# Optimization experiments

Measured on AMD Instinct MI355X. Metric: run time of the kernel, lower is better.

Reference implementation:

```python
import jax, jax.numpy as jnp
import numpy as np

D_MODEL = 1024
H = 16
DK = 64
DV = 64
D_OUT = 1024
SEQ = 1024
BATCH = 4


def setup_inputs() -> dict:
    key = jax.random.key(0)
    ks = jax.random.split(key, 11)
    s = 0.02
    return {
        "query": jax.random.normal(ks[0], (SEQ, BATCH, D_MODEL), jnp.float32),
        "key": jax.random.normal(ks[1], (SEQ, BATCH, D_MODEL), jnp.float32),
        "value": jax.random.normal(ks[2], (SEQ, BATCH, D_MODEL), jnp.float32),
        "Wq": jax.random.normal(ks[3], (D_MODEL, H * DK), jnp.float32) * s,
        "bq": jnp.zeros((H * DK,), jnp.float32),
        "Wk": jax.random.normal(ks[4], (D_MODEL, H * DK), jnp.float32) * s,
        "bk": jnp.zeros((H * DK,), jnp.float32),
        "Wv": jax.random.normal(ks[5], (D_MODEL, H * DV), jnp.float32) * s,
        "bv": jnp.zeros((H * DV,), jnp.float32),
        "Wo": jax.random.normal(ks[6], (H * DV, D_OUT), jnp.float32) * s,
        "bo": jnp.zeros((D_OUT,), jnp.float32),
    }


def reference(query, key, value, Wq, bq, Wk, bk, Wv, bv, Wo, bo):
    S, B, _ = query.shape
    # projections (seq-first layout, like the torch module)
    q = query @ Wq + bq            # (S, B, H*DK)
    k = key @ Wk + bk              # (S, B, H*DK)
    v = value @ Wv + bv            # (S, B, H*DV)
    # view + transpose(0, 2): (S, B, H, d) -> (H, B, S, d)
    q = jnp.transpose(q.reshape(S, B, H, DK), (2, 1, 0, 3))
    k = jnp.transpose(k.reshape(S, B, H, DK), (2, 1, 0, 3))
    v = jnp.transpose(v.reshape(S, B, H, DV), (2, 1, 0, 3))
    # scaled dot-product attention, full logits materialized as in the original
    logits = jnp.einsum("hbsd,hbtd->hbst", q, k) / jnp.sqrt(jnp.float32(DK))
    attn = jax.nn.softmax(logits, axis=-1)            # (H, B, S, S)
    ctx = jnp.einsum("hbst,hbtd->hbsd", attn, v)       # (H, B, S, DV)
    # transpose(0, 2) back and merge heads: (S, B, H*DV)
    ctx = jnp.transpose(ctx, (2, 1, 0, 3)).reshape(S, B, H * DV)
    out = ctx @ Wo + bo                               # (S, B, D_OUT)
    return (out, attn)
```

## Files before the change

kernel.cpp:

```cpp
#include <hip/hip_runtime.h>


typedef unsigned short u16;
typedef unsigned int u32;
typedef short short8v __attribute__((ext_vector_type(8)));
typedef short short4v __attribute__((ext_vector_type(4)));
typedef float f32x4 __attribute__((ext_vector_type(4)));

__device__ __forceinline__ u16 f2bf(float f) {
    u32 u = __builtin_bit_cast(u32, f);
    u += 0x7fffu + ((u >> 16) & 1u);
    return (u16)(u >> 16);
}
__device__ __forceinline__ f32x4 mfma_bf16(short8v a, short8v b, f32x4 c) {
    return __builtin_amdgcn_mfma_f32_16x16x32_bf16(a, b, c, 0, 0, 0);
}
__device__ __forceinline__ void gload16(const void* g, void* l) {
    __builtin_amdgcn_global_load_lds((const __attribute__((address_space(1))) u32*)g,
                                     (__attribute__((address_space(3))) u32*)l, 16, 0, 0);
}

__global__ __launch_bounds__(256) void cvt_inputs(const float* __restrict__ X0,
                                                  const float* __restrict__ X1,
                                                  const float* __restrict__ X2,
                                                  u16* __restrict__ Y0, u16* __restrict__ Y1,
                                                  u16* __restrict__ Y2) {
    const float* X; u16* Y;
    switch (blockIdx.y) {
        case 0: X = X0; Y = Y0; break;
        case 1: X = X1; Y = Y1; break;
        default: X = X2; Y = Y2; break;
    }
    const int tid = blockIdx.x * 256 + threadIdx.x;
    const int row = tid >> 7;
    const int c = tid & 127;
    const float4* s4 = reinterpret_cast<const float4*>(X + (size_t)row * 1024 + c * 8);
    float4 v0 = s4[0], v1 = s4[1];
    short8v p;
    p[0] = (short)f2bf(v0.x); p[1] = (short)f2bf(v0.y);
    p[2] = (short)f2bf(v0.z); p[3] = (short)f2bf(v0.w);
    p[4] = (short)f2bf(v1.x); p[5] = (short)f2bf(v1.y);
    p[6] = (short)f2bf(v1.z); p[7] = (short)f2bf(v1.w);
    const int dc = (c & ~7) | ((c ^ row) & 7);
    *reinterpret_cast<short8v*>(Y + (size_t)row * 1024 + dc * 8) = p;
}

__global__ __launch_bounds__(256) void cvt_transpose_w4(const float* __restrict__ W0,
                                                        const float* __restrict__ W1,
                                                        const float* __restrict__ W2,
                                                        const float* __restrict__ W3,
                                                        u16* __restrict__ T0, u16* __restrict__ T1,
                                                        u16* __restrict__ T2, u16* __restrict__ T3) {
    __shared__ u16 T[64][72];
    const float* W; u16* Wt;
    switch (blockIdx.y) {
        case 0: W = W0; Wt = T0; break;
        case 1: W = W1; Wt = T1; break;
        case 2: W = W2; Wt = T2; break;
        default: W = W3; Wt = T3; break;
    }
    const int n0 = (blockIdx.x & 15) << 6;
    const int k0 = (blockIdx.x >> 4) << 6;
    const int t = threadIdx.x;
    const int r = t >> 2;
    const int c = t & 3;
    const float4* src = reinterpret_cast<const float4*>(W + (size_t)(k0 + r) * 1024 + n0 + c * 16);
#pragma unroll
    for (int j = 0; j < 4; ++j) {
        float4 v = src[j];
        T[c * 16 + j * 4 + 0][r] = f2bf(v.x);
        T[c * 16 + j * 4 + 1][r] = f2bf(v.y);
        T[c * 16 + j * 4 + 2][r] = f2bf(v.z);
        T[c * 16 + j * 4 + 3][r] = f2bf(v.w);
    }
    __syncthreads();
    const int s = r & 7;
    const int p0 = (c << 1) ^ s;
    const int p1 = ((c << 1) | 1) ^ s;
    u16* base = Wt + (size_t)(n0 + r) * 1024 + k0;
    *reinterpret_cast<short8v*>(base + p0 * 8) = *reinterpret_cast<const short8v*>(&T[r][c * 16]);
    *reinterpret_cast<short8v*>(base + p1 * 8) = *reinterpret_cast<const short8v*>(&T[r][c * 16 + 8]);
}

__global__ __launch_bounds__(256, 3) void gemm_qkv(const u16* __restrict__ Abq,
                                                   const u16* __restrict__ Abk,
                                                   const u16* __restrict__ Abv,
                                                   const u16* __restrict__ Wtq,
                                                   const u16* __restrict__ Wtk,
                                                   const u16* __restrict__ Wtv,
                                                   const float* __restrict__ bq,
                                                   const float* __restrict__ bk,
                                                   const float* __restrict__ bv,
                                                   u16* __restrict__ dq, u16* __restrict__ dk,
                                                   u16* __restrict__ dv) {
    __shared__ u16 As[128][64];
    __shared__ u16 Bs[128][64];
    const u16* Ab; const u16* Wt; const float* bias; u16* dst;
    switch (blockIdx.z) {
        case 0: Ab = Abq; Wt = Wtq; bias = bq; dst = dq; break;
        case 1: Ab = Abk; Wt = Wtk; bias = bk; dst = dk; break;
        default: Ab = Abv; Wt = Wtv; bias = bv; dst = dv; break;
    }
    const int m0 = blockIdx.y << 7;
    const int n0 = blockIdx.x << 7;
    const int t = threadIdx.x;
    const int lane = t & 63;
    const int w = t >> 6;
    const int wr = (w >> 1) << 6;
    const int wc = (w & 1) << 6;
    const int l15 = lane & 15, lg = lane >> 4;

    const u16* ga = Ab + (size_t)(m0 + w * 32 + (lane >> 3)) * 1024 + (lane & 7) * 8;
    const u16* gb = Wt + (size_t)(n0 + w * 32 + (lane >> 3)) * 1024 + (lane & 7) * 8;

    f32x4 acc[4][4] = {};

    for (int kt = 0; kt < 16; ++kt) {
        const int k0 = kt << 6;
        if (kt) __syncthreads();
#pragma unroll
        for (int j = 0; j < 4; ++j) {
            gload16(ga + j * 8 * 1024 + k0, &As[w * 32 + j * 8][0]);
            gload16(gb + j * 8 * 1024 + k0, &Bs[w * 32 + j * 8][0]);
        }
        __syncthreads();
#pragma unroll
        for (int kk = 0; kk < 2; ++kk) {
            short8v a[4], b[4];
#pragma unroll
            for (int m = 0; m < 4; ++m) {
                const int row = wr + m * 16 + l15;
                a[m] = *reinterpret_cast<const short8v*>(&As[row][(((kk << 2) | lg) ^ (row & 7)) << 3]);
            }
#pragma unroll
            for (int n = 0; n < 4; ++n) {
                const int row = wc + n * 16 + l15;
                b[n] = *reinterpret_cast<const short8v*>(&Bs[row][(((kk << 2) | lg) ^ (row & 7)) << 3]);
            }
#pragma unroll
            for (int m = 0; m < 4; ++m)
#pragma unroll
                for (int n = 0; n < 4; ++n)
                    acc[m][n] = mfma_bf16(a[m], b[n], acc[m][n]);
        }
    }

#pragma unroll
    for (int n = 0; n < 4; ++n) {
        const int c = n0 + wc + n * 16 + l15;
        const float bvv = bias[c];
        const int h = c >> 6, d = c & 63;
#pragma unroll
        for (int m = 0; m < 4; ++m) {
#pragma unroll
            for (int r = 0; r < 4; ++r) {
                const int mi = m0 + wr + m * 16 + lg * 4 + r;
                const int s = mi >> 2, bb = mi & 3;
                dst[(size_t)(((h << 2) + bb) << 16) + (s << 6) + d] = f2bf(acc[m][n][r] + bvv);
            }
        }
    }
}

__global__ __launch_bounds__(256) void transpose_v(const u16* __restrict__ vb,
                                                   u16* __restrict__ vtb) {
    __shared__ u16 T[64][72];
    const int hb = blockIdx.y;
    const int s0 = blockIdx.x << 6;
    const u16* src = vb + (size_t)hb * 65536;
    u16* dst = vtb + (size_t)hb * 65536;
    const int t = threadIdx.x;
    const int r = t >> 2;
    const int c = (t & 3) << 4;
    short8v v0 = *reinterpret_cast<const short8v*>(src + (size_t)(s0 + r) * 64 + c);
    short8v v1 = *reinterpret_cast<const short8v*>(src + (size_t)(s0 + r) * 64 + c + 8);
#pragma unroll
    for (int j = 0; j < 8; ++j) T[c + j][r] = (u16)v0[j];
#pragma unroll
    for (int j = 0; j < 8; ++j) T[c + 8 + j][r] = (u16)v1[j];
    __syncthreads();
    *reinterpret_cast<short8v*>(dst + (size_t)r * 1024 + s0 + c)     = *reinterpret_cast<const short8v*>(&T[r][c]);
    *reinterpret_cast<short8v*>(dst + (size_t)r * 1024 + s0 + c + 8) = *reinterpret_cast<const short8v*>(&T[r][c + 8]);
}

__global__ __launch_bounds__(512, 4) void attn_kernel(const u16* __restrict__ qb,
                                                      const u16* __restrict__ kb,
                                                      const u16* __restrict__ vtb,
                                                      float* __restrict__ attn_out,
                                                      u16* __restrict__ ctxb) {
    __shared__ float Sm[16 * 1024];
    char* Sb = (char*)Sm;
    const int hb = blockIdx.y;
    const int q0 = blockIdx.x << 4;
    const int h = hb >> 2, b = hb & 3;
    const int t = threadIdx.x;
    const int lane = t & 63, w = t >> 6;
    const int l15 = lane & 15, lg = lane >> 4;

    const u16* Q = qb + (size_t)hb * 65536;
    const u16* K = kb + (size_t)hb * 65536;
    const u16* VT = vtb + (size_t)hb * 65536;

    short8v aq[2];
#pragma unroll
    for (int kh = 0; kh < 2; ++kh)
        aq[kh] = *reinterpret_cast<const short8v*>(Q + (q0 + l15) * 64 + kh * 32 + lg * 8);

#pragma unroll
    for (int n = 0; n < 8; ++n) {
        const int tcol = w * 128 + n * 16 + l15;
        f32x4 acc = {};
#pragma unroll
        for (int kh = 0; kh < 2; ++kh) {
            short8v bk = *reinterpret_cast<const short8v*>(K + tcol * 64 + kh * 32 + lg * 8);
            acc = mfma_bf16(aq[kh], bk, acc);
        }
#pragma unroll
        for (int r = 0; r < 4; ++r) {
            const int row = lg * 4 + r;
            *(float*)(Sb + (row << 12) + ((tcol << 2) ^ ((row & 7) << 4))) = acc[r] * 0.125f;
        }
    }
    __syncthreads();

#pragma unroll
    for (int rr = 0; rr < 2; ++rr) {
        const int r = w * 2 + rr;
        const int swz = (r & 7) << 4;
        f32x4 vv[4];
#pragma unroll
        for (int j = 0; j < 4; ++j)
            vv[j] = *(const f32x4*)(Sb + (r << 12) + (((lane * 4 + j * 256) << 2) ^ swz));
        float mx = -1e30f;
#pragma unroll
        for (int j = 0; j < 4; ++j)
#pragma unroll
            for (int i = 0; i < 4; ++i) mx = fmaxf(mx, vv[j][i]);
#pragma unroll
        for (int o = 1; o < 64; o <<= 1) mx = fmaxf(mx, __shfl_xor(mx, o, 64));
        float sum = 0.f;
#pragma unroll
        for (int j = 0; j < 4; ++j)
#pragma unroll
            for (int i = 0; i < 4; ++i) { vv[j][i] = __expf(vv[j][i] - mx); sum += vv[j][i]; }
#pragma unroll
        for (int o = 1; o < 64; o <<= 1) sum += __shfl_xor(sum, o, 64);
        const float inv = 1.0f / sum;
        float* grow = attn_out + (((size_t)(hb << 10) + q0 + r) << 10);
#pragma unroll
        for (int j = 0; j < 4; ++j) {
            f32x4 p = vv[j] * inv;
            *reinterpret_cast<f32x4*>(grow + lane * 4 + j * 256) = p;
            short4v pk;
            pk[0] = (short)f2bf(p[0]); pk[1] = (short)f2bf(p[1]);
            pk[2] = (short)f2bf(p[2]); pk[3] = (short)f2bf(p[3]);
            *(short4v*)(Sb + (r << 12) + (((lane * 4 + j * 256) << 1) ^ swz)) = pk;
        }
    }
    __syncthreads();

    f32x4 cacc[4] = {};
#pragma unroll
    for (int kt = 0; kt < 4; ++kt) {
        const int kcol = w * 128 + kt * 32 + lg * 8;
        short8v ap = *(const short8v*)(Sb + (l15 << 12) + ((kcol << 1) ^ ((l15 & 7) << 4)));
#pragma unroll
        for (int n = 0; n < 4; ++n) {
            short8v bv = *reinterpret_cast<const short8v*>(VT + (size_t)(n * 16 + l15) * 1024 + kcol);
            cacc[n] = mfma_bf16(ap, bv, cacc[n]);
        }
    }
    __syncthreads();

    float* part = Sm;
#pragma unroll
    for (int n = 0; n < 4; ++n)
#pragma unroll
        for (int r = 0; r < 4; ++r)
            part[w * 1088 + (lg * 4 + r) * 68 + n * 16 + l15] = cacc[n][r];
    __syncthreads();
    if (t < 256) {
        const int rrow = t >> 4;
        const int c0 = (t & 15) << 2;
        f32x4 s = {};
#pragma unroll
        for (int ww = 0; ww < 8; ++ww)
            s += *reinterpret_cast<const f32x4*>(&part[ww * 1088 + rrow * 68 + c0]);
        short4v o;
        o[0] = (short)f2bf(s[0]); o[1] = (short)f2bf(s[1]);
        o[2] = (short)f2bf(s[2]); o[3] = (short)f2bf(s[3]);
        const int mi = ((q0 + rrow) << 2) + b;
        const int off = h * 64 + (((c0 >> 3) ^ (mi & 7)) << 3) + (c0 & 7);
        *reinterpret_cast<short4v*>(ctxb + (size_t)mi * 1024 + off) = o;
    }
}

__global__ __launch_bounds__(256, 2) void gemm_out(const u16* __restrict__ ctxb,
                                                   const u16* __restrict__ Wto,
                                                   const float* __restrict__ bo,
                                                   float* __restrict__ out) {
    __shared__ u16 As[64][64];
    __shared__ u16 Bs[128][64];
    const int m0 = blockIdx.y << 6;
    const int n0 = blockIdx.x << 7;
    const int t = threadIdx.x;
    const int lane = t & 63;
    const int w = t >> 6;
    const int wr = (w >> 1) << 5;
    const int wc = (w & 1) << 6;
    const int l15 = lane & 15, lg = lane >> 4;

    const u16* ga = ctxb + (size_t)(m0 + w * 16 + (lane >> 3)) * 1024 + (lane & 7) * 8;
    const u16* gb = Wto + (size_t)(n0 + w * 32 + (lane >> 3)) * 1024 + (lane & 7) * 8;

    f32x4 acc[2][4] = {};

    for (int kt = 0; kt < 16; ++kt) {
        const int k0 = kt << 6;
        if (kt) __syncthreads();
#pragma unroll
        for (int j = 0; j < 2; ++j)
            gload16(ga + j * 8 * 1024 + k0, &As[w * 16 + j * 8][0]);
#pragma unroll
        for (int j = 0; j < 4; ++j)
            gload16(gb + j * 8 * 1024 + k0, &Bs[w * 32 + j * 8][0]);
        __syncthreads();
#pragma unroll
        for (int kk = 0; kk < 2; ++kk) {
            short8v a[2], b[4];
#pragma unroll
            for (int m = 0; m < 2; ++m) {
                const int row = wr + m * 16 + l15;
                a[m] = *reinterpret_cast<const short8v*>(&As[row][(((kk << 2) | lg) ^ (row & 7)) << 3]);
            }
#pragma unroll
            for (int n = 0; n < 4; ++n) {
                const int row = wc + n * 16 + l15;
                b[n] = *reinterpret_cast<const short8v*>(&Bs[row][(((kk << 2) | lg) ^ (row & 7)) << 3]);
            }
#pragma unroll
            for (int m = 0; m < 2; ++m)
#pragma unroll
                for (int n = 0; n < 4; ++n)
                    acc[m][n] = mfma_bf16(a[m], b[n], acc[m][n]);
        }
    }

#pragma unroll
    for (int n = 0; n < 4; ++n) {
        const int c = n0 + wc + n * 16 + l15;
        const float bvv = bo[c];
#pragma unroll
        for (int m = 0; m < 2; ++m)
#pragma unroll
            for (int r = 0; r < 4; ++r) {
                const int mi = m0 + wr + m * 16 + lg * 4 + r;
                out[(size_t)mi * 1024 + c] = acc[m][n][r] + bvv;
            }
    }
}

extern "C" void kernel_launch(void* const* d_in, const int* in_sizes, int n_in,
                              void* d_out, int out_size, void* d_ws, size_t ws_size,
                              hipStream_t stream) {
    const float* query = (const float*)d_in[0];
    const float* key   = (const float*)d_in[1];
    const float* value = (const float*)d_in[2];
    const float* Wq = (const float*)d_in[3];
    const float* bq = (const float*)d_in[4];
    const float* Wk = (const float*)d_in[5];
    const float* bk = (const float*)d_in[6];
    const float* Wv = (const float*)d_in[7];
    const float* bv = (const float*)d_in[8];
    const float* Wo = (const float*)d_in[9];
    const float* bo = (const float*)d_in[10];

    char* ws = (char*)d_ws;
    u16* Wtq  = (u16*)(ws);
    u16* Wtk  = (u16*)(ws + ((size_t)2 << 20));
    u16* Wtv  = (u16*)(ws + ((size_t)4 << 20));
    u16* Wto  = (u16*)(ws + ((size_t)6 << 20));
    u16* qb   = (u16*)(ws + ((size_t)8 << 20));
    u16* kb   = (u16*)(ws + ((size_t)16 << 20));
    u16* vb   = (u16*)(ws + ((size_t)24 << 20));
    u16* vtb  = (u16*)(ws + ((size_t)32 << 20));
    u16* ctxb = (u16*)(ws + ((size_t)24 << 20));
    u16* Abq  = (u16*)(ws + ((size_t)40 << 20));
    u16* Abk  = (u16*)(ws + ((size_t)48 << 20));
    u16* Abv  = (u16*)(ws + ((size_t)56 << 20));

    float* out  = (float*)d_out;
    float* attn = out + (size_t)4 * 1024 * 1024;

    cvt_transpose_w4<<<dim3(256, 4), 256, 0, stream>>>(Wq, Wk, Wv, Wo, Wtq, Wtk, Wtv, Wto);
    cvt_inputs<<<dim3(2048, 3), 256, 0, stream>>>(query, key, value, Abq, Abk, Abv);

    gemm_qkv<<<dim3(8, 32, 3), 256, 0, stream>>>(Abq, Abk, Abv, Wtq, Wtk, Wtv,
                                                 bq, bk, bv, qb, kb, vb);

    transpose_v<<<dim3(16, 64), 256, 0, stream>>>(vb, vtb);

    attn_kernel<<<dim3(64, 64), 512, 0, stream>>>(qb, kb, vtb, attn, ctxb);

    gemm_out<<<dim3(8, 64), 256, 0, stream>>>(ctxb, Wto, bo, out);
}
```

Measured before the change: 504.5 us.

## Split attention into QK-softmax kernel and separate tiled P·V GEMM

The fused attention kernel is split in two. The first kernel computes logits and softmax, writes the fp32 attention output, and also writes a bf16 copy of P to global memory with a swizzled layout. A new tiled GEMM kernel then computes P·V using LDS tiles with 128-row reuse, instead of each 16-row block re-reading all of V^T from global memory and doing a cross-wave reduction. The cost is an extra 128MB bf16 round trip for P and one more kernel launch, in exchange for better V reuse and lower LDS pressure in the softmax kernel.

```diff
diff --git a/kernel.cpp b/kernel.cpp
--- a/kernel.cpp
+++ b/kernel.cpp
@@ -179,27 +179,28 @@
 #pragma unroll
     for (int j = 0; j < 8; ++j) T[c + 8 + j][r] = (u16)v1[j];
     __syncthreads();
-    *reinterpret_cast<short8v*>(dst + (size_t)r * 1024 + s0 + c)     = *reinterpret_cast<const short8v*>(&T[r][c]);
-    *reinterpret_cast<short8v*>(dst + (size_t)r * 1024 + s0 + c + 8) = *reinterpret_cast<const short8v*>(&T[r][c + 8]);
-}
-
-__global__ __launch_bounds__(512, 4) void attn_kernel(const u16* __restrict__ qb,
-                                                      const u16* __restrict__ kb,
-                                                      const u16* __restrict__ vtb,
-                                                      float* __restrict__ attn_out,
-                                                      u16* __restrict__ ctxb) {
+    const int r7 = r & 7;
+    const int ch0 = (s0 + c) >> 3;
+    const int d0 = (ch0 & ~7) | ((ch0 ^ r7) & 7);
+    const int d1 = ((ch0 + 1) & ~7) | (((ch0 + 1) ^ r7) & 7);
+    *reinterpret_cast<short8v*>(dst + (size_t)r * 1024 + d0 * 8) = *reinterpret_cast<const short8v*>(&T[r][c]);
+    *reinterpret_cast<short8v*>(dst + (size_t)r * 1024 + d1 * 8) = *reinterpret_cast<const short8v*>(&T[r][c + 8]);
+}
+
+__global__ __launch_bounds__(512, 2) void attn_qks(const u16* __restrict__ qb,
+                                                   const u16* __restrict__ kb,
+                                                   float* __restrict__ attn_out,
+                                                   u16* __restrict__ Pg) {
     __shared__ float Sm[16 * 1024];
     char* Sb = (char*)Sm;
     const int hb = blockIdx.y;
     const int q0 = blockIdx.x << 4;
-    const int h = hb >> 2, b = hb & 3;
     const int t = threadIdx.x;
     const int lane = t & 63, w = t >> 6;
     const int l15 = lane & 15, lg = lane >> 4;
 
     const u16* Q = qb + (size_t)hb * 65536;
     const u16* K = kb + (size_t)hb * 65536;
-    const u16* VT = vtb + (size_t)hb * 65536;
 
     short8v aq[2];
 #pragma unroll
@@ -246,7 +247,10 @@
 #pragma unroll
         for (int o = 1; o < 64; o <<= 1) sum += __shfl_xor(sum, o, 64);
         const float inv = 1.0f / sum;
-        float* grow = attn_out + (((size_t)(hb << 10) + q0 + r) << 10);
+        const int q = q0 + r;
+        float* grow = attn_out + (((size_t)(hb << 10) + q) << 10);
+        u16* prow = Pg + ((size_t)hb << 20) + ((size_t)q << 10);
+        const int q7 = q & 7;
 #pragma unroll
         for (int j = 0; j < 4; ++j) {
             f32x4 p = vv[j] * inv;
@@ -254,44 +258,79 @@
             short4v pk;
             pk[0] = (short)f2bf(p[0]); pk[1] = (short)f2bf(p[1]);
             pk[2] = (short)f2bf(p[2]); pk[3] = (short)f2bf(p[3]);
-            *(short4v*)(Sb + (r << 12) + (((lane * 4 + j * 256) << 1) ^ swz)) = pk;
-        }
-    }
-    __syncthreads();
-
-    f32x4 cacc[4] = {};
-#pragma unroll
-    for (int kt = 0; kt < 4; ++kt) {
-        const int kcol = w * 128 + kt * 32 + lg * 8;
-        short8v ap = *(const short8v*)(Sb + (l15 << 12) + ((kcol << 1) ^ ((l15 & 7) << 4)));
-#pragma unroll
-        for (int n = 0; n < 4; ++n) {
-            short8v bv = *reinterpret_cast<const short8v*>(VT + (size_t)(n * 16 + l15) * 1024 + kcol);
-            cacc[n] = mfma_bf16(ap, bv, cacc[n]);
-        }
-    }
-    __syncthreads();
-
-    float* part = Sm;
-#pragma unroll
-    for (int n = 0; n < 4; ++n)
-#pragma unroll
-        for (int r = 0; r < 4; ++r)
-            part[w * 1088 + (lg * 4 + r) * 68 + n * 16 + l15] = cacc[n][r];
-    __syncthreads();
-    if (t < 256) {
-        const int rrow = t >> 4;
-        const int c0 = (t & 15) << 2;
-        f32x4 s = {};
-#pragma unroll
-        for (int ww = 0; ww < 8; ++ww)
-            s += *reinterpret_cast<const f32x4*>(&part[ww * 1088 + rrow * 68 + c0]);
-        short4v o;
-        o[0] = (short)f2bf(s[0]); o[1] = (short)f2bf(s[1]);
-        o[2] = (short)f2bf(s[2]); o[3] = (short)f2bf(s[3]);
-        const int mi = ((q0 + rrow) << 2) + b;
-        const int off = h * 64 + (((c0 >> 3) ^ (mi & 7)) << 3) + (c0 & 7);
-        *reinterpret_cast<short4v*>(ctxb + (size_t)mi * 1024 + off) = o;
+            const int col = lane * 4 + j * 256;
+            const int ch = col >> 3;
+            const int dch = (ch & ~7) | ((ch ^ q7) & 7);
+            *reinterpret_cast<short4v*>(prow + dch * 8 + (col & 7)) = pk;
+        }
+    }
+}
+
+__global__ __launch_bounds__(256, 3) void gemm_pv(const u16* __restrict__ Pg,
+                                                  const u16* __restrict__ vtb,
+                                                  u16* __restrict__ ctxb) {
+    __shared__ u16 As[128][64];
+    __shared__ u16 Bs[64][64];
+    const int q0 = blockIdx.x << 7;
+    const int hb = blockIdx.y;
+    const int h = hb >> 2, b = hb & 3;
+    const int t = threadIdx.x;
+    const int lane = t & 63;
+    const int w = t >> 6;
+    const int wr = w << 5;
+    const int l15 = lane & 15, lg = lane >> 4;
+
+    const u16* ga = Pg + ((size_t)hb << 20) + (size_t)(q0 + w * 32 + (lane >> 3)) * 1024 + (lane & 7) * 8;
+    const u16* gb = vtb + ((size_t)hb << 16) + (size_t)(w * 16 + (lane >> 3)) * 1024 + (lane & 7) * 8;
+
+    f32x4 acc[2][4] = {};
+
+    for (int kt = 0; kt < 16; ++kt) {
+        const int k0 = kt << 6;
+        if (kt) __syncthreads();
+#pragma unroll
+        for (int j = 0; j < 4; ++j)
+            gload16(ga + j * 8 * 1024 + k0, &As[w * 32 + j * 8][0]);
+#pragma unroll
+        for (int j = 0; j < 2; ++j)
+            gload16(gb + j * 8 * 1024 + k0, &Bs[w * 16 + j * 8][0]);
+        __syncthreads();
+#pragma unroll
+        for (int kk = 0; kk < 2; ++kk) {
+            short8v a[2], b[4];
+#pragma unroll
+            for (int m = 0; m < 2; ++m) {
+                const int row = wr + m * 16 + l15;
+                a[m] = *reinterpret_cast<const short8v*>(&As[row][(((kk << 2) | lg) ^ (row & 7)) << 3]);
+            }
+#pragma unroll
+            for (int n = 0; n < 4; ++n) {
+                const int row = n * 16 + l15;
+                b[n] = *reinterpret_cast<const short8v*>(&Bs[row][(((kk << 2) | lg) ^ (row & 7)) << 3]);
+            }
+#pragma unroll
+            for (int m = 0; m < 2; ++m)
+#pragma unroll
+                for (int n = 0; n < 4; ++n)
+                    acc[m][n] = mfma_bf16(a[m], b[n], acc[m][n]);
+        }
+    }
+
+#pragma unroll
+    for (int n = 0; n < 4; ++n) {
+        const int dv = n * 16 + l15;
+        const int c = (h << 6) + dv;
+        const int ch = c >> 3;
+        const int cl = c & 7;
+#pragma unroll
+        for (int m = 0; m < 2; ++m)
+#pragma unroll
+            for (int rI = 0; rI < 4; ++rI) {
+                const int q = q0 + wr + m * 16 + lg * 4 + rI;
+                const int mi = (q << 2) + b;
+                const int dch = (ch & ~7) | ((ch ^ mi) & 7);
+                ctxb[(size_t)mi * 1024 + dch * 8 + cl] = f2bf(acc[m][n][rI]);
+            }
     }
 }
 
@@ -388,6 +427,7 @@
     u16* Abq  = (u16*)(ws + ((size_t)40 << 20));
     u16* Abk  = (u16*)(ws + ((size_t)48 << 20));
     u16* Abv  = (u16*)(ws + ((size_t)56 << 20));
+    u16* Pg   = (u16*)(ws + ((size_t)64 << 20));
 
     float* out  = (float*)d_out;
     float* attn = out + (size_t)4 * 1024 * 1024;
@@ -400,7 +440,9 @@
 
     transpose_v<<<dim3(16, 64), 256, 0, stream>>>(vb, vtb);
 
-    attn_kernel<<<dim3(64, 64), 512, 0, stream>>>(qb, kb, vtb, attn, ctxb);
+    attn_qks<<<dim3(64, 64), 512, 0, stream>>>(qb, kb, attn, Pg);
+
+    gemm_pv<<<dim3(8, 64), 256, 0, stream>>>(Pg, vtb, ctxb);
 
     gemm_out<<<dim3(8, 64), 256, 0, stream>>>(ctxb, Wto, bo, out);
 }
```

Result: no change. 507.1 us (+0.5%).
